# Performance work log

Measured on AMD Instinct MI355X. Metric: run time of the kernel, lower is better.

## Reference

```python
import jax, jax.numpy as jnp
import numpy as np

B, T, C, H = 4, 2048, 1024, 16
HD = C // H


def setup_inputs() -> dict:
    key = jax.random.key(0)
    k1, k2, k3, k4 = jax.random.split(key, 4)
    x = jax.random.normal(k1, (B, T, C), dtype=jnp.float32)
    pad_mask = jnp.ones((B, T), dtype=jnp.int32)
    # Linear weights stored as (in, out); torch Linear uses W.T so math is identical.
    w_attn = jax.random.normal(k2, (C, 3 * C), dtype=jnp.float32) * (1.0 / np.sqrt(C))
    w_proj = jax.random.normal(k3, (C, C), dtype=jnp.float32) * (1.0 / np.sqrt(C))
    b_proj = jax.random.normal(k4, (C,), dtype=jnp.float32) * 0.01
    return {"x": x, "pad_mask": pad_mask, "w_attn": w_attn, "w_proj": w_proj, "b_proj": b_proj}


def reference(x, pad_mask, w_attn, w_proj, b_proj):
    Bx, Tx, Cx = x.shape
    hd = Cx // H
    qkv = x @ w_attn                                  # (B,T,3C)
    q, k, v = jnp.split(qkv, 3, axis=2)
    # (B,T,C) -> (B,H,T,hd)
    q = q.reshape(Bx, Tx, H, hd).transpose(0, 2, 1, 3)
    k = k.reshape(Bx, Tx, H, hd).transpose(0, 2, 1, 3)
    v = v.reshape(Bx, Tx, H, hd).transpose(0, 2, 1, 3)
    att = jnp.einsum('bhqd,bhkd->bhqk', q, k) * (1.0 / np.sqrt(hd))
    causal = jnp.tril(jnp.ones((Tx, Tx), dtype=bool))[None, None]       # (1,1,T,T)
    keep = causal & (pad_mask[:, None, None, :] != 0)                   # (B,1,T,T) broadcast
    att = jnp.where(keep, att, -jnp.inf)
    att = jax.nn.softmax(att, axis=-1)
    # dropout p=0.0 (eval) -> identity
    y = jnp.einsum('bhqk,bhkd->bhqd', att, v)
    y = y.transpose(0, 2, 1, 3).reshape(Bx, Tx, Cx)
    return y @ w_proj + b_proj
```

## Files before the change

### kernel.cpp

```cpp
#include <hip/hip_runtime.h>
#include <hip/hip_bf16.h>


using short8  = __attribute__((ext_vector_type(8))) short;
using float4_ = __attribute__((ext_vector_type(4))) float;

#define Bb   4
#define Tt   2048
#define Cc   1024
#define Hh   16
#define HDd  64

__device__ __forceinline__ float bf2f(unsigned short u) {
    union { float f; unsigned int i; } x; x.i = ((unsigned int)u) << 16; return x.f;
}
__device__ __forceinline__ unsigned short f2bf(float f) {
    union { float f; unsigned int i; } x; x.f = f;
    unsigned int r = x.i + 0x7fff + ((x.i >> 16) & 1);
    return (unsigned short)(r >> 16);
}
__device__ __forceinline__ float4_ bmfma(short8 a, short8 b, float4_ c) {
    return __builtin_amdgcn_mfma_f32_16x16x32_bf16(a, b, c, 0, 0, 0);
}
__device__ __forceinline__ void gl2lds16(const unsigned short* g, unsigned short* l) {
    __builtin_amdgcn_global_load_lds(
        (const __attribute__((address_space(1))) void*)g,
        (__attribute__((address_space(3))) void*)l, 16, 0, 0);
}

__global__ __launch_bounds__(256) void convert_f32_bf16(
    const float* __restrict__ in, unsigned short* __restrict__ out)
{
    size_t idx = ((size_t)blockIdx.x * 256 + threadIdx.x) * 8;
    float4_ f0 = *(const float4_*)&in[idx];
    float4_ f1 = *(const float4_*)&in[idx + 4];
    short8 h;
    h[0] = (short)f2bf(f0[0]); h[1] = (short)f2bf(f0[1]);
    h[2] = (short)f2bf(f0[2]); h[3] = (short)f2bf(f0[3]);
    h[4] = (short)f2bf(f1[0]); h[5] = (short)f2bf(f1[1]);
    h[6] = (short)f2bf(f1[2]); h[7] = (short)f2bf(f1[3]);
    *(short8*)&out[idx] = h;
}

__global__ __launch_bounds__(256) void transpose_f32_bf16(
    const float* __restrict__ in, unsigned short* __restrict__ out,
    int R, int Ccols)
{
    __shared__ unsigned short tile[32][33];
    int c0 = blockIdx.x * 32, r0 = blockIdx.y * 32;
    int tx = threadIdx.x & 31, ty = threadIdx.x >> 5;
    for (int o = 0; o < 32; o += 8)
        tile[ty + o][tx] = f2bf(in[(size_t)(r0 + ty + o) * Ccols + c0 + tx]);
    __syncthreads();
    for (int o = 0; o < 32; o += 8)
        out[(size_t)(c0 + ty + o) * R + r0 + tx] = tile[tx][ty + o];
}

#define GBK 64

__device__ __forceinline__ void gemm128_main(
    const unsigned short* __restrict__ A, const unsigned short* __restrict__ Bt,
    int K, int m0, int n0,
    unsigned short* As, unsigned short* Bs, float4_ acc[4][4])
{
    int tid  = threadIdx.x;
    int wave = tid >> 6, lane = tid & 63;
    int wm = (wave >> 1) * 64, wn = (wave & 1) * 64;
    int lr = lane & 15, lg = lane >> 4;
    int srow = tid >> 3;
    int scol = (tid & 7) * 8;

    for (int k0 = 0; k0 < K; k0 += GBK) {
        #pragma unroll
        for (int j = 0; j < 4; j++) {
            int row = j * 32 + srow;
            gl2lds16(&A [(size_t)(m0 + row) * K + k0 + scol], &As[row * GBK + scol]);
            gl2lds16(&Bt[(size_t)(n0 + row) * K + k0 + scol], &Bs[row * GBK + scol]);
        }
        __syncthreads();
        #pragma unroll
        for (int ks = 0; ks < GBK; ks += 32) {
            short8 af[4], bf[4];
            #pragma unroll
            for (int i = 0; i < 4; i++) {
                af[i] = *(const short8*)&As[(wm + i * 16 + lr) * GBK + ks + lg * 8];
                bf[i] = *(const short8*)&Bs[(wn + i * 16 + lr) * GBK + ks + lg * 8];
            }
            #pragma unroll
            for (int i = 0; i < 4; i++)
                #pragma unroll
                for (int j = 0; j < 4; j++)
                    acc[i][j] = bmfma(af[i], bf[j], acc[i][j]);
        }
        __syncthreads();
    }
}

__global__ __launch_bounds__(256) void gemm_qkv(
    const unsigned short* __restrict__ A,
    const unsigned short* __restrict__ Bt,
    unsigned short* __restrict__ Q,
    unsigned short* __restrict__ Ko,
    unsigned short* __restrict__ V)
{
    __shared__ unsigned short As[128 * GBK];
    __shared__ unsigned short Bs[128 * GBK];
    int m0 = blockIdx.x * 128, n0 = blockIdx.y * 128;
    float4_ acc[4][4] = {};
    gemm128_main(A, Bt, 1024, m0, n0, As, Bs, acc);

    int lane = threadIdx.x & 63, wave = threadIdx.x >> 6;
    int wm = (wave >> 1) * 64, wn = (wave & 1) * 64;
    int lr = lane & 15, lg = lane >> 4;
    #pragma unroll
    for (int i = 0; i < 4; i++)
        #pragma unroll
        for (int j = 0; j < 4; j++) {
            int n = n0 + wn + 16 * j + lr;
            int which = n >> 10;
            int c = n & 1023;
            int h = c >> 6, d = c & 63;
            unsigned short* dst = (which == 0) ? Q : ((which == 1) ? Ko : V);
            float sc2 = (which == 0) ? 0.125f : 1.0f;
            #pragma unroll
            for (int r = 0; r < 4; r++) {
                int m = m0 + wm + 16 * i + lg * 4 + r;
                int b = m >> 11, t = m & 2047;
                dst[(((size_t)(b * Hh + h) * Tt) + t) * HDd + d] = f2bf(acc[i][j][r] * sc2);
            }
        }
}

__global__ __launch_bounds__(256) void gemm_proj(
    const unsigned short* __restrict__ A,
    const unsigned short* __restrict__ Bt,
    const float* __restrict__ bias,
    float* __restrict__ Out)
{
    __shared__ unsigned short As[128 * GBK];
    __shared__ unsigned short Bs[128 * GBK];
    int m0 = blockIdx.x * 128, n0 = blockIdx.y * 128;
    float4_ acc[4][4] = {};
    gemm128_main(A, Bt, 1024, m0, n0, As, Bs, acc);

    int lane = threadIdx.x & 63, wave = threadIdx.x >> 6;
    int wm = (wave >> 1) * 64, wn = (wave & 1) * 64;
    int lr = lane & 15, lg = lane >> 4;
    #pragma unroll
    for (int i = 0; i < 4; i++)
        #pragma unroll
        for (int j = 0; j < 4; j++) {
            int n = n0 + wn + 16 * j + lr;
            float bv = bias[n];
            #pragma unroll
            for (int r = 0; r < 4; r++) {
                int m = m0 + wm + 16 * i + lg * 4 + r;
                Out[(size_t)m * 1024 + n] = acc[i][j][r] + bv;
            }
        }
}

#define DPAD 72

__global__ __launch_bounds__(256) void attn_fwd(
    const unsigned short* __restrict__ Q,
    const unsigned short* __restrict__ Kg,
    const unsigned short* __restrict__ Vg,
    const int* __restrict__ pad,
    unsigned short* __restrict__ Y)
{
    __shared__ unsigned short smem[128 * DPAD];
    unsigned short* Kt = smem;
    unsigned short* Vt = smem + 64 * DPAD;

    int flat = blockIdx.x;
    int qb = 31 - (flat >> 6);
    int bh = flat & 63;
    int b  = bh >> 4, h = bh & 15;
    const size_t base = (size_t)bh * Tt * HDd;
    int tid  = threadIdx.x;
    int wave = tid >> 6, lane = tid & 63;
    int lr = lane & 15, lg = lane >> 4;
    int q0 = qb * 64 + wave * 16;
    unsigned short* Pw = &Kt[wave * 16 * DPAD];
    const int* padRow = pad + b * Tt;

    short8 qf0 = *(const short8*)&Q[base + (size_t)(q0 + lr) * HDd + lg * 8];
    short8 qf1 = *(const short8*)&Q[base + (size_t)(q0 + lr) * HDd + 32 + lg * 8];

    float m_i[4], l_i[4];
    float4_ o_acc[4];
    #pragma unroll
    for (int r = 0; r < 4; r++) { m_i[r] = -1e30f; l_i[r] = 0.f; }
    #pragma unroll
    for (int dt = 0; dt < 4; dt++) o_acc[dt] = (float4_){0.f, 0.f, 0.f, 0.f};

    for (int kt = 0; kt <= qb; kt++) {
        int k0 = kt * 64;
        {
            int r = tid >> 2, cbase = (tid & 3) * 8;
            #pragma unroll
            for (int half = 0; half < 2; half++) {
                int c = cbase + half * 32;
                *(short8*)&Kt[r * DPAD + c] =
                    *(const short8*)&Kg[base + (size_t)(k0 + r) * HDd + c];
                alignas(16) unsigned short tmp[8];
                *(short8*)tmp = *(const short8*)&Vg[base + (size_t)(k0 + r) * HDd + c];
                #pragma unroll
                for (int j = 0; j < 8; j++) {
                    int d = c + j;
                    Vt[d * DPAD + ((((r >> 3) ^ (d >> 3)) << 3) | (r & 7))] = tmp[j];
                }
            }
        }
        __syncthreads();

        float4_ s[4];
        #pragma unroll
        for (int nt = 0; nt < 4; nt++) {
            short8 kf0 = *(const short8*)&Kt[(nt * 16 + lr) * DPAD + lg * 8];
            short8 kf1 = *(const short8*)&Kt[(nt * 16 + lr) * DPAD + 32 + lg * 8];
            float4_ a = (float4_){0.f, 0.f, 0.f, 0.f};
            a = bmfma(qf0, kf0, a);
            a = bmfma(qf1, kf1, a);
            s[nt] = a;
        }
        #pragma unroll
        for (int nt = 0; nt < 4; nt++) {
            int key = k0 + nt * 16 + lr;
            bool keep_k = padRow[key] != 0;
            #pragma unroll
            for (int r = 0; r < 4; r++) {
                int qrow = q0 + lg * 4 + r;
                float sv = s[nt][r];
                if (!keep_k || key > qrow) sv = -1e30f;
                s[nt][r] = sv;
            }
        }
        float mn[4], alpha[4];
        #pragma unroll
        for (int r = 0; r < 4; r++) {
            float v = fmaxf(fmaxf(s[0][r], s[1][r]), fmaxf(s[2][r], s[3][r]));
            #pragma unroll
            for (int off = 1; off < 16; off <<= 1)
                v = fmaxf(v, __shfl_xor(v, off, 64));
            float m_new = fmaxf(m_i[r], v);
            alpha[r] = __expf(m_i[r] - m_new);
            mn[r] = m_new;
        }
        float rsum[4] = {0.f, 0.f, 0.f, 0.f};
        #pragma unroll
        for (int nt = 0; nt < 4; nt++)
            #pragma unroll
            for (int r = 0; r < 4; r++) {
                float p = __expf(s[nt][r] - mn[r]);
                s[nt][r] = p;
                rsum[r] += p;
            }
        #pragma unroll
        for (int r = 0; r < 4; r++) {
            float v = rsum[r];
            #pragma unroll
            for (int off = 1; off < 16; off <<= 1)
                v += __shfl_xor(v, off, 64);
            l_i[r] = l_i[r] * alpha[r] + v;
            m_i[r] = mn[r];
        }

        __syncthreads();

        #pragma unroll
        for (int nt = 0; nt < 4; nt++)
            #pragma unroll
            for (int r = 0; r < 4; r++)
                Pw[(lg * 4 + r) * DPAD + nt * 16 + lr] = f2bf(s[nt][r]);
        #pragma unroll
        for (int dt = 0; dt < 4; dt++)
            #pragma unroll
            for (int r = 0; r < 4; r++)
                o_acc[dt][r] *= alpha[r];
        short8 pf0 = *(const short8*)&Pw[lr * DPAD + lg * 8];
        short8 pf1 = *(const short8*)&Pw[lr * DPAD + 32 + lg * 8];
        #pragma unroll
        for (int dt = 0; dt < 4; dt++) {
            int d = dt * 16 + lr;
            short8 vf0 = *(const short8*)&Vt[d * DPAD + ((lg ^ (d >> 3)) << 3)];
            short8 vf1 = *(const short8*)&Vt[d * DPAD + (((lg + 4) ^ (d >> 3)) << 3)];
            o_acc[dt] = bmfma(pf0, vf0, o_acc[dt]);
            o_acc[dt] = bmfma(pf1, vf1, o_acc[dt]);
        }
        __syncthreads();
    }

    #pragma unroll
    for (int dt = 0; dt < 4; dt++)
        #pragma unroll
        for (int r = 0; r < 4; r++) {
            int qrow = q0 + lg * 4 + r;
            Y[((size_t)b * Tt + qrow) * Cc + h * HDd + dt * 16 + lr] =
                f2bf(o_acc[dt][r] / l_i[r]);
        }
}

extern "C" void kernel_launch(void* const* d_in, const int* in_sizes, int n_in,
                              void* d_out, int out_size, void* d_ws, size_t ws_size,
                              hipStream_t stream)
{
    const float* x      = (const float*)d_in[0];
    const int*   pad    = (const int*)d_in[1];
    const float* w_attn = (const float*)d_in[2];
    const float* w_proj = (const float*)d_in[3];
    const float* b_proj = (const float*)d_in[4];
    float*       out    = (float*)d_out;

    unsigned short* Wta = (unsigned short*)d_ws;
    unsigned short* Wtp = Wta + (size_t)3072 * 1024;
    unsigned short* Xb  = Wtp + (size_t)1024 * 1024;
    unsigned short* Yb  = Xb;
    unsigned short* Qb  = Xb + (size_t)8192 * 1024;
    unsigned short* Kb  = Qb + (size_t)Bb * Hh * Tt * HDd;
    unsigned short* Vb  = Kb + (size_t)Bb * Hh * Tt * HDd;

    convert_f32_bf16<<<dim3(4096), 256, 0, stream>>>(x, Xb);
    transpose_f32_bf16<<<dim3(3072 / 32, 1024 / 32), 256, 0, stream>>>(w_attn, Wta, 1024, 3072);
    transpose_f32_bf16<<<dim3(1024 / 32, 1024 / 32), 256, 0, stream>>>(w_proj, Wtp, 1024, 1024);
    gemm_qkv<<<dim3(8192 / 128, 3072 / 128), 256, 0, stream>>>(Xb, Wta, Qb, Kb, Vb);
    attn_fwd<<<dim3(2048), 256, 0, stream>>>(Qb, Kb, Vb, pad, Yb);
    gemm_proj<<<dim3(8192 / 128, 1024 / 128), 256, 0, stream>>>(Yb, Wtp, b_proj, out);
}
```

Measured before the change: 332.7 us.

## Write V transposed from QKV GEMM, prefetch K/V tiles in registers, ballot pad mask

```diff
diff --git a/kernel.cpp b/kernel.cpp
--- a/kernel.cpp
+++ b/kernel.cpp
@@ -61,7 +61,7 @@
 __device__ __forceinline__ void gemm128_main(
     const unsigned short* __restrict__ A, const unsigned short* __restrict__ Bt,
     int K, int m0, int n0,
-    unsigned short* As, unsigned short* Bs, float4_ acc[4][4])
+    unsigned short* As, unsigned short* Bs, float4_ acc[4][4], bool swapT)
 {
     int tid  = threadIdx.x;
     int wave = tid >> 6, lane = tid & 63;
@@ -86,11 +86,19 @@
                 af[i] = *(const short8*)&As[(wm + i * 16 + lr) * GBK + ks + lg * 8];
                 bf[i] = *(const short8*)&Bs[(wn + i * 16 + lr) * GBK + ks + lg * 8];
             }
-            #pragma unroll
-            for (int i = 0; i < 4; i++)
-                #pragma unroll
-                for (int j = 0; j < 4; j++)
-                    acc[i][j] = bmfma(af[i], bf[j], acc[i][j]);
+            if (!swapT) {
+                #pragma unroll
+                for (int i = 0; i < 4; i++)
+                    #pragma unroll
+                    for (int j = 0; j < 4; j++)
+                        acc[i][j] = bmfma(af[i], bf[j], acc[i][j]);
+            } else {
+                #pragma unroll
+                for (int i = 0; i < 4; i++)
+                    #pragma unroll
+                    for (int j = 0; j < 4; j++)
+                        acc[i][j] = bmfma(bf[i], af[j], acc[i][j]);
+            }
         }
         __syncthreads();
     }
@@ -106,29 +114,47 @@
     __shared__ unsigned short As[128 * GBK];
     __shared__ unsigned short Bs[128 * GBK];
     int m0 = blockIdx.x * 128, n0 = blockIdx.y * 128;
+    bool vblk = (n0 >= 2048);
     float4_ acc[4][4] = {};
-    gemm128_main(A, Bt, 1024, m0, n0, As, Bs, acc);
+    gemm128_main(A, Bt, 1024, m0, n0, As, Bs, acc, vblk);
 
     int lane = threadIdx.x & 63, wave = threadIdx.x >> 6;
     int wm = (wave >> 1) * 64, wn = (wave & 1) * 64;
     int lr = lane & 15, lg = lane >> 4;
-    #pragma unroll
-    for (int i = 0; i < 4; i++)
-        #pragma unroll
-        for (int j = 0; j < 4; j++) {
-            int n = n0 + wn + 16 * j + lr;
-            int which = n >> 10;
-            int c = n & 1023;
-            int h = c >> 6, d = c & 63;
-            unsigned short* dst = (which == 0) ? Q : ((which == 1) ? Ko : V);
-            float sc2 = (which == 0) ? 0.125f : 1.0f;
-            #pragma unroll
-            for (int r = 0; r < 4; r++) {
-                int m = m0 + wm + 16 * i + lg * 4 + r;
+    if (!vblk) {
+        #pragma unroll
+        for (int i = 0; i < 4; i++)
+            #pragma unroll
+            for (int j = 0; j < 4; j++) {
+                int n = n0 + wn + 16 * j + lr;
+                int which = n >> 10;
+                int c = n & 1023;
+                int h = c >> 6, d = c & 63;
+                unsigned short* dst = (which == 0) ? Q : Ko;
+                float sc2 = (which == 0) ? 0.125f : 1.0f;
+                #pragma unroll
+                for (int r = 0; r < 4; r++) {
+                    int m = m0 + wm + 16 * i + lg * 4 + r;
+                    int b = m >> 11, t = m & 2047;
+                    dst[(((size_t)(b * Hh + h) * Tt) + t) * HDd + d] = f2bf(acc[i][j][r] * sc2);
+                }
+            }
+    } else {
+        #pragma unroll
+        for (int i = 0; i < 4; i++)
+            #pragma unroll
+            for (int j = 0; j < 4; j++) {
+                int m = m0 + wm + 16 * j + lr;
                 int b = m >> 11, t = m & 2047;
-                dst[(((size_t)(b * Hh + h) * Tt) + t) * HDd + d] = f2bf(acc[i][j][r] * sc2);
-            }
-        }
+                #pragma unroll
+                for (int r = 0; r < 4; r++) {
+                    int n = n0 + wn + 16 * i + lg * 4 + r;
+                    int c = n - 2048;
+                    int h = c >> 6, d = c & 63;
+                    V[(((size_t)(b * Hh + h) * HDd) + d) * Tt + t] = f2bf(acc[i][j][r]);
+                }
+            }
+    }
 }
 
 __global__ __launch_bounds__(256) void gemm_proj(
@@ -141,7 +167,7 @@
     __shared__ unsigned short Bs[128 * GBK];
     int m0 = blockIdx.x * 128, n0 = blockIdx.y * 128;
     float4_ acc[4][4] = {};
-    gemm128_main(A, Bt, 1024, m0, n0, As, Bs, acc);
+    gemm128_main(A, Bt, 1024, m0, n0, As, Bs, acc, false);
 
     int lane = threadIdx.x & 63, wave = threadIdx.x >> 6;
     int wm = (wave >> 1) * 64, wn = (wave & 1) * 64;
@@ -185,6 +211,9 @@
     unsigned short* Pw = &Kt[wave * 16 * DPAD];
     const int* padRow = pad + b * Tt;
 
+    int sr = tid >> 2;
+    int sc = (tid & 3) * 8;
+
     short8 qf0 = *(const short8*)&Q[base + (size_t)(q0 + lr) * HDd + lg * 8];
     short8 qf1 = *(const short8*)&Q[base + (size_t)(q0 + lr) * HDd + 32 + lg * 8];
 
@@ -195,25 +224,30 @@
     #pragma unroll
     for (int dt = 0; dt < 4; dt++) o_acc[dt] = (float4_){0.f, 0.f, 0.f, 0.f};
 
+    const unsigned short* kp0 = &Kg[base + (size_t)sr * HDd + sc];
+    const unsigned short* vp0 = &Vg[base + (size_t)sr * Tt + sc];
+    short8 kr0 = *(const short8*)kp0;
+    short8 kr1 = *(const short8*)(kp0 + 32);
+    short8 vr0 = *(const short8*)vp0;
+    short8 vr1 = *(const short8*)(vp0 + 32);
+
     for (int kt = 0; kt <= qb; kt++) {
         int k0 = kt * 64;
-        {
-            int r = tid >> 2, cbase = (tid & 3) * 8;
-            #pragma unroll
-            for (int half = 0; half < 2; half++) {
-                int c = cbase + half * 32;
-                *(short8*)&Kt[r * DPAD + c] =
-                    *(const short8*)&Kg[base + (size_t)(k0 + r) * HDd + c];
-                alignas(16) unsigned short tmp[8];
-                *(short8*)tmp = *(const short8*)&Vg[base + (size_t)(k0 + r) * HDd + c];
-                #pragma unroll
-                for (int j = 0; j < 8; j++) {
-                    int d = c + j;
-                    Vt[d * DPAD + ((((r >> 3) ^ (d >> 3)) << 3) | (r & 7))] = tmp[j];
-                }
-            }
-        }
-        __syncthreads();
+        *(short8*)&Kt[sr * DPAD + sc]      = kr0;
+        *(short8*)&Kt[sr * DPAD + sc + 32] = kr1;
+        *(short8*)&Vt[sr * DPAD + sc]      = vr0;
+        *(short8*)&Vt[sr * DPAD + sc + 32] = vr1;
+        int pvld = padRow[k0 + lane];
+        unsigned long long pm = __ballot(pvld != 0);
+        __syncthreads();
+        if (kt < qb) {
+            const unsigned short* kp = &Kg[base + (size_t)(k0 + 64 + sr) * HDd + sc];
+            const unsigned short* vp = &Vg[base + (size_t)sr * Tt + k0 + 64 + sc];
+            kr0 = *(const short8*)kp;
+            kr1 = *(const short8*)(kp + 32);
+            vr0 = *(const short8*)vp;
+            vr1 = *(const short8*)(vp + 32);
+        }
 
         float4_ s[4];
         #pragma unroll
@@ -225,16 +259,24 @@
             a = bmfma(qf1, kf1, a);
             s[nt] = a;
         }
-        #pragma unroll
-        for (int nt = 0; nt < 4; nt++) {
-            int key = k0 + nt * 16 + lr;
-            bool keep_k = padRow[key] != 0;
-            #pragma unroll
-            for (int r = 0; r < 4; r++) {
-                int qrow = q0 + lg * 4 + r;
-                float sv = s[nt][r];
-                if (!keep_k || key > qrow) sv = -1e30f;
-                s[nt][r] = sv;
+        if (kt == qb) {
+            #pragma unroll
+            for (int nt = 0; nt < 4; nt++) {
+                int key = k0 + nt * 16 + lr;
+                bool kpv = (pm >> (nt * 16 + lr)) & 1ull;
+                #pragma unroll
+                for (int r = 0; r < 4; r++) {
+                    int qrow = q0 + lg * 4 + r;
+                    if (!kpv || key > qrow) s[nt][r] = -1e30f;
+                }
+            }
+        } else if (pm != ~0ull) {
+            #pragma unroll
+            for (int nt = 0; nt < 4; nt++) {
+                bool kpv = (pm >> (nt * 16 + lr)) & 1ull;
+                #pragma unroll
+                for (int r = 0; r < 4; r++)
+                    s[nt][r] = kpv ? s[nt][r] : -1e30f;
             }
         }
         float mn[4], alpha[4];
@@ -284,8 +326,8 @@
         #pragma unroll
         for (int dt = 0; dt < 4; dt++) {
             int d = dt * 16 + lr;
-            short8 vf0 = *(const short8*)&Vt[d * DPAD + ((lg ^ (d >> 3)) << 3)];
-            short8 vf1 = *(const short8*)&Vt[d * DPAD + (((lg + 4) ^ (d >> 3)) << 3)];
+            short8 vf0 = *(const short8*)&Vt[d * DPAD + lg * 8];
+            short8 vf1 = *(const short8*)&Vt[d * DPAD + 32 + lg * 8];
             o_acc[dt] = bmfma(pf0, vf0, o_acc[dt]);
             o_acc[dt] = bmfma(pf1, vf1, o_acc[dt]);
         }
```

New measurement: 336.1 us. No clear change (+1.0%).
